# Kernel optimization log

Measured on AMD Instinct MI355X. Metric: run time of the kernel, lower is better.

Reference implementation:

```python
import jax, jax.numpy as jnp
import numpy as np

H, U = 64, 64  # matrix-completion patch size; system size is (H*U)^2 = 4096^2


def svtC(X, tau):
    # Singular value thresholding: soft-threshold singular values by tau.
    u, s, vt = jnp.linalg.svd(X, full_matrices=False)
    return (u * jax.nn.relu(s - tau)) @ vt


def setup_inputs() -> dict:
    key = jax.random.key(0)
    ks = jax.random.split(key, 12)
    x = jax.random.normal(ks[0], (H, U), jnp.float32)
    L = jax.random.normal(ks[1], (H, U), jnp.float32)
    entries_mask = jax.random.randint(ks[2], (H, U), 0, 2).astype(bool)
    # D_tilda: symmetric PSD (HU, HU) smoothness operator so the system is well-conditioned
    M = jax.random.normal(ks[3], (H * U, H * U), jnp.float32)
    D_tilda = (M @ M.T) / jnp.float32(H * U)
    th_P = jax.random.normal(ks[4], (H, U), jnp.float32)
    v = jax.random.normal(ks[5], (), jnp.float32)
    coef_gamma = jax.random.uniform(ks[6], (), jnp.float32)
    neta = jax.random.uniform(ks[7], (), jnp.float32)
    lamda1 = jax.random.uniform(ks[8], (), jnp.float32)
    lamda2 = jax.random.uniform(ks[9], (), jnp.float32)
    rho = jax.random.uniform(ks[10], (), jnp.float32) + jnp.float32(0.1)
    S = jax.random.normal(ks[11], (H, H), jnp.float32) / np.float32(np.sqrt(H))
    return {"x": x, "L": L, "entries_mask": entries_mask, "D_tilda": D_tilda,
            "th_P": th_P, "v": v, "coef_gamma": coef_gamma, "neta": neta,
            "lamda1": lamda1, "lamda2": lamda2, "rho": rho, "S": S}


def reference(x, L, entries_mask, D_tilda, th_P, v, coef_gamma, neta,
              lamda1, lamda2, rho, S):
    tau = jax.nn.sigmoid(v) * coef_gamma
    # Q_tilda = diag(vec(mask)); S_tilda = kron(I_U, S^T S)
    q = entries_mask.astype(jnp.float32).reshape(-1)  # (HU,)
    StS = S.T @ S                                      # (H, H)
    S_tilda = jnp.kron(jnp.eye(U, dtype=jnp.float32), StS)  # (HU, HU)
    eye = jnp.eye(H * U, dtype=jnp.float32)
    A = jnp.diag(q) + lamda1 * D_tilda + lamda2 * S_tilda + rho * eye
    vec = rho * (L - th_P) + jnp.where(entries_mask, x, jnp.float32(0.0))
    # Original uses explicit dense inverse followed by matvec
    Xtmp = (jnp.linalg.inv(A) @ vec.reshape(-1)).reshape(H, U)
    Ltmp = svtC(Xtmp + th_P, tau)
    Ptmp = th_P + neta * (Xtmp - Ltmp)
    return Ltmp, Ptmp
```

## Files before the change

### kernel.cpp

```cpp
#include <hip/hip_runtime.h>
#include <cstddef>

#define HU    4096
#define NBLK  256
#define NTHR  512
#define MAXIT 100
#define TOL2  1e-7f

#define WS_STS  0
#define WS_DINV 4096
#define WS_R0   8192
#define WS_U0   12288
#define WS_W    16384
#define WS_X    24576
#define WS_DEL  28672
#define WS_BAR  (WS_DEL + (MAXIT + 2) * 64)
#define WS_FLAG (WS_BAR + 8 * 16)
#define WS_END  (WS_FLAG + 1)

typedef _Float16 half4v __attribute__((ext_vector_type(4)));

__device__ __forceinline__ float fastrcp(float x) {
  float r; asm("v_rcp_f32 %0, %1" : "=v"(r) : "v"(x)); return r;
}
__device__ __forceinline__ float fastsqrt(float x) {
  float r; asm("v_sqrt_f32 %0, %1" : "=v"(r) : "v"(x)); return r;
}
__device__ __forceinline__ float fastrsq(float x) {
  float r; asm("v_rsq_f32 %0, %1" : "=v"(r) : "v"(x)); return r;
}

__device__ __forceinline__ float waveReduce(float v) {
#pragma unroll
  for (int off = 32; off > 0; off >>= 1) v += __shfl_xor(v, off, 64);
  return v;
}

__device__ __forceinline__ float blockSum(float v, float* red) {
  v = waveReduce(v);
  if ((threadIdx.x & 63) == 0) red[threadIdx.x >> 6] = v;
  __syncthreads();
  float s = 0.f;
#pragma unroll
  for (int i = 0; i < 8; ++i) s += red[i];
  __syncthreads();
  return s;
}

__device__ __forceinline__ void gsync(unsigned* cnt, unsigned* flag, unsigned gen) {
  __syncthreads();
  if (threadIdx.x == 0) {
    __threadfence();
    __hip_atomic_fetch_add(&cnt[(blockIdx.x & 7) * 16], 1u,
                           __ATOMIC_RELEASE, __HIP_MEMORY_SCOPE_AGENT);
    if (blockIdx.x == 0) {
      const unsigned target = gen * NBLK;
      for (;;) {
        unsigned s = 0;
#pragma unroll
        for (int i = 0; i < 8; ++i)
          s += __hip_atomic_load(&cnt[i * 16], __ATOMIC_RELAXED, __HIP_MEMORY_SCOPE_AGENT);
        if (s >= target) break;
        __builtin_amdgcn_s_sleep(1);
      }
      __hip_atomic_store(flag, gen, __ATOMIC_RELEASE, __HIP_MEMORY_SCOPE_AGENT);
    } else {
      while (__hip_atomic_load(flag, __ATOMIC_RELAXED, __HIP_MEMORY_SCOPE_AGENT) < gen)
        __builtin_amdgcn_s_sleep(1);
    }
    __threadfence();
  }
  __syncthreads();
}

__global__ void __launch_bounds__(NTHR, 1)
cg_solve_kernel(const float* __restrict__ x_in, const float* __restrict__ L_in,
                const int* __restrict__ mask, const float* __restrict__ D,
                const float* __restrict__ thP, const float* __restrict__ S,
                const float* __restrict__ l1p, const float* __restrict__ l2p,
                const float* __restrict__ rhop, float* __restrict__ ws)
{
  __shared__ __align__(16) float u_l[HU];
  __shared__ __align__(16) _Float16 Dh[16 * HU];
  __shared__ float red[8];
  unsigned* cnt  = (unsigned*)(ws + WS_BAR);
  unsigned* flag = (unsigned*)(ws + WS_FLAG);
  const float* sts = ws + WS_STS;
  const float lam1 = *l1p, lam2 = *l2p, rho = *rhop;
  const int tid = threadIdx.x, b = blockIdx.x;
  const int wv = tid >> 6, lane = tid & 63;
  unsigned gen = 0;

  const int gtid = b * NTHR + tid;
  if (gtid < HU) {
    const int a = gtid >> 6, c = gtid & 63;
    float acc = 0.f, sdiag = 0.f;
    for (int h = 0; h < 64; ++h) {
      const float sa = S[h * 64 + a], sc = S[h * 64 + c];
      acc = fmaf(sa, sc, acc);
      sdiag = fmaf(sc, sc, sdiag);
    }
    ws[WS_STS + gtid] = acc;
    const float q = mask[gtid] ? 1.f : 0.f;
    const float diag = q + rho + lam1 * D[(size_t)gtid * (HU + 1)] + lam2 * sdiag;
    const float bb = rho * (L_in[gtid] - thP[gtid]) + (mask[gtid] ? x_in[gtid] : 0.f);
    const float di = 1.f / diag;
    ws[WS_DINV + gtid] = di;
    ws[WS_R0 + gtid] = bb;
    ws[WS_U0 + gtid] = bb * di;
  }

  {
    const float4* __restrict__ Dg = (const float4*)(D + (size_t)b * 16 * HU);
    half4v* __restrict__ Dh4 = (half4v*)Dh;
    for (int o = tid; o < 16 * HU / 4; o += NTHR) {
      const float4 dv = Dg[o];
      half4v h;
      h[0] = (_Float16)dv.x; h[1] = (_Float16)dv.y;
      h[2] = (_Float16)dv.z; h[3] = (_Float16)dv.w;
      Dh4[o] = h;
    }
  }
  gsync(cnt, flag, ++gen);

  float r_reg[8], s_reg[8], dinv_reg[8];
  float acc0 = 0.f;
#pragma unroll
  for (int m = 0; m < 8; ++m) {
    const int i = tid + m * NTHR;
    const float rv = ws[WS_R0 + i], uv = ws[WS_U0 + i];
    r_reg[m] = rv; u_l[i] = uv; dinv_reg[m] = ws[WS_DINV + i];
    s_reg[m] = 0.f;
  }
  __syncthreads();
#pragma unroll
  for (int m = 0; m < 8; ++m) acc0 = fmaf(r_reg[m], u_l[tid + m * NTHR], acc0);
  const float gamma0 = blockSum(acc0, red);

  float p_arr[8], x_arr[8];
#pragma unroll
  for (int m = 0; m < 8; ++m) { p_arr[m] = 0.f; x_arr[m] = 0.f; }

  const int row0 = b * 16 + wv * 2;
  const int iq = row0 >> 6, j0 = row0 & 63;
  const float4* __restrict__ u4 = (const float4*)u_l;
  const float m0 = mask[row0] ? 1.f : 0.f;
  const float m1 = mask[row0 + 1] ? 1.f : 0.f;
  const float sts0 = sts[j0 * 64 + lane];
  const float sts1 = sts[j0 * 64 + 64 + lane];
  const float dex0 = D[(size_t)row0 * (HU + 1)];
  const float dex1 = D[(size_t)(row0 + 1) * (HU + 1)];
  const float diagf0 = m0 + rho + lam1 * (dex0 - (float)(_Float16)dex0);
  const float diagf1 = m1 + rho + lam1 * (dex1 - (float)(_Float16)dex1);
  const half4v* __restrict__ H0 = (const half4v*)(Dh + (size_t)(wv * 2) * HU);
  const half4v* __restrict__ H1 = H0 + (HU / 4);

  float gamma = gamma0, gamma_prev = 1.f, alpha_prev = 1.f;
  for (int k = 0; k < MAXIT; ++k) {
    float* __restrict__ wbuf = ws + WS_W + (k & 1) * HU;
    {
      float acc_a = 0.f, acc_b = 0.f;
#pragma unroll
      for (int it = 0; it < 16; ++it) {
        const float4 uu = u4[it * 64 + lane];
        const half4v d0 = H0[it * 64 + lane];
        const half4v d1 = H1[it * 64 + lane];
        acc_a = fmaf((float)d0[0], uu.x, acc_a); acc_a = fmaf((float)d0[1], uu.y, acc_a);
        acc_a = fmaf((float)d0[2], uu.z, acc_a); acc_a = fmaf((float)d0[3], uu.w, acc_a);
        acc_b = fmaf((float)d1[0], uu.x, acc_b); acc_b = fmaf((float)d1[1], uu.y, acc_b);
        acc_b = fmaf((float)d1[2], uu.z, acc_b); acc_b = fmaf((float)d1[3], uu.w, acc_b);
      }
      const float us = u_l[iq * 64 + lane];
      float t0 = fmaf(lam1, acc_a, lam2 * (sts0 * us));
      float t1 = fmaf(lam1, acc_b, lam2 * (sts1 * us));
      t0 = waveReduce(t0);
      t1 = waveReduce(t1);
      const float u0v = u_l[row0], u1v = u_l[row0 + 1];
      const float w0 = t0 + diagf0 * u0v;
      const float w1 = t1 + diagf1 * u1v;
      if (lane == 0) {
        wbuf[row0] = w0;
        wbuf[row0 + 1] = w1;
        red[wv] = fmaf(w0, u0v, w1 * u1v);
      }
      __syncthreads();
      if (tid == 0) {
        float s = 0.f;
#pragma unroll
        for (int k2 = 0; k2 < 8; ++k2) s += red[k2];
        atomicAdd(&ws[WS_DEL + k * 64 + (b & 63)], s);
      }
    }
    gsync(cnt, flag, ++gen);

    const float dk = waveReduce(ws[WS_DEL + k * 64 + lane]);
    const float beta  = (k == 0) ? 0.f : gamma * fastrcp(gamma_prev);
    const float denom = (k == 0) ? dk  : (dk - beta * gamma * fastrcp(alpha_prev));
    const float alpha = gamma * fastrcp(denom);

    float acc = 0.f;
#pragma unroll
    for (int m = 0; m < 8; ++m) {
      const int i = tid + m * NTHR;
      const float uold = u_l[i];
      const float wvv = wbuf[i];
      const float sv = (k == 0) ? wvv : fmaf(beta, s_reg[m], wvv);
      s_reg[m] = sv;
      const float rv = fmaf(-alpha, sv, r_reg[m]);
      r_reg[m] = rv;
      const float uv = rv * dinv_reg[m];
      u_l[i] = uv;
      acc = fmaf(rv, uv, acc);
      const float pk = (k == 0) ? uold : fmaf(beta, p_arr[m], uold);
      p_arr[m] = pk;
      x_arr[m] = fmaf(alpha, pk, x_arr[m]);
    }
    const float gnext = blockSum(acc, red);

    gamma_prev = gamma;
    alpha_prev = alpha;
    gamma = gnext;
    if (!(gnext > TOL2 * gamma0)) break;
  }

  if (b == 0) {
#pragma unroll
    for (int m = 0; m < 8; ++m) ws[WS_X + tid + m * NTHR] = x_arr[m];
  }
}


#define SWP 6
#define S_W 68

__device__ __forceinline__ float red16(float x) {
  int t;
  t = __builtin_amdgcn_update_dpp(0, __float_as_int(x), 0x128, 0xF, 0xF, false);
  x += __int_as_float(t);
  t = __builtin_amdgcn_update_dpp(0, __float_as_int(x), 0x124, 0xF, 0xF, false);
  x += __int_as_float(t);
  t = __builtin_amdgcn_update_dpp(0, __float_as_int(x), 0x122, 0xF, 0xF, false);
  x += __int_as_float(t);
  t = __builtin_amdgcn_update_dpp(0, __float_as_int(x), 0x121, 0xF, 0xF, false);
  x += __int_as_float(t);
  return x;
}

__global__ void __launch_bounds__(512)
svt_kernel(const float* __restrict__ thP, const float* __restrict__ vp,
           const float* __restrict__ cgp, const float* __restrict__ netap,
           const float* __restrict__ ws, float* __restrict__ out)
{
  const float* xsol = ws + WS_X;
  __shared__ __align__(16) float Wl[64 * S_W];
  __shared__ __align__(16) float Yr[64 * S_W];
  __shared__ __align__(16) float T1[64 * S_W];
  __shared__ __align__(16) float Wr[64 * S_W];
  __shared__ float g_s[64];
  __shared__ float red[8];
  const int tid = threadIdx.x;

  float t0acc = 0.f;
  for (int o = tid; o < 4096; o += 512) {
    const int r = o >> 6, c = o & 63;
    const float y = xsol[o] + thP[o];
    Wl[c * S_W + r] = y;
    Yr[r * S_W + c] = y;
    t0acc = fmaf(y, y, t0acc);
  }
  const float T0 = blockSum(t0acc, red);
  const float thr = 1.6e-10f * T0 * T0;

  const int m = tid >> 4;
  const int sub = tid & 15;
  int p = (m == 0) ? 63 : m;
  int q = (m == 0) ? 0  : 63 - m;

  for (int sweep = 0; sweep < SWP; ++sweep) {
    float offacc = 0.f;
    for (int rnd = 0; rnd < 63; ++rnd) {
      float4* wp = (float4*)(Wl + p * S_W) + sub;
      float4* wq = (float4*)(Wl + q * S_W) + sub;
      const float4 a = *wp, bb = *wq;
      float dpp = fmaf(a.x, a.x, fmaf(a.y, a.y, fmaf(a.z, a.z, a.w * a.w)));
      float dqq = fmaf(bb.x, bb.x, fmaf(bb.y, bb.y, fmaf(bb.z, bb.z, bb.w * bb.w)));
      float dpq = fmaf(a.x, bb.x, fmaf(a.y, bb.y, fmaf(a.z, bb.z, a.w * bb.w)));
      dpp = red16(dpp); dqq = red16(dqq); dpq = red16(dpq);
      offacc = fmaf(dpq, dpq, offacc);
      if (dpq * dpq > 1e-14f * dpp * dqq) {
        const float th = (dqq - dpp) * 0.5f * fastrcp(dpq);
        const float sg = (th >= 0.f) ? 1.f : -1.f;
        const float t  = sg * fastrcp(fabsf(th) + fastsqrt(fmaf(th, th, 1.f)));
        const float c1 = fastrsq(fmaf(t, t, 1.f));
        const float s1 = t * c1;
        float4 na, nb;
        na.x = c1 * a.x - s1 * bb.x;  nb.x = s1 * a.x + c1 * bb.x;
        na.y = c1 * a.y - s1 * bb.y;  nb.y = s1 * a.y + c1 * bb.y;
        na.z = c1 * a.z - s1 * bb.z;  nb.z = s1 * a.z + c1 * bb.z;
        na.w = c1 * a.w - s1 * bb.w;  nb.w = s1 * a.w + c1 * bb.w;
        *wp = na; *wq = nb;
      }
      if (m) { p = (p + 1 == 63) ? 0 : p + 1; }
      q = (q + 1 == 63) ? 0 : q + 1;
      __syncthreads();
    }
    const float tot = blockSum(offacc, red);
    if (sweep >= 3 && tot < thr) break;
  }

  if (tid < 64) {
    const float4* wc = (const float4*)(Wl + tid * S_W);
    float nn = 0.f;
#pragma unroll
    for (int i2 = 0; i2 < 16; ++i2) {
      const float4 u = wc[i2];
      nn = fmaf(u.x, u.x, fmaf(u.y, u.y, fmaf(u.z, u.z, fmaf(u.w, u.w, nn))));
    }
    const float sv = sqrtf(nn);
    const float tau = (*cgp) / (1.f + expf(-(*vp)));
    g_s[tid] = (sv > tau) ? (sv - tau) / (sv * nn) : 0.f;
  }
  __syncthreads();

  const int j = tid & 63;
  const int ib = tid >> 6;

#pragma unroll
  for (int mm = 0; mm < 8; ++mm) {
    const int k = ib + 8 * mm;
    const float4* wcol = (const float4*)(Wl + k * S_W);
    float acc = 0.f;
#pragma unroll
    for (int i4 = 0; i4 < 16; ++i4) {
      const float4 wv = wcol[i4];
      acc = fmaf(wv.x, Yr[(4 * i4 + 0) * S_W + j], acc);
      acc = fmaf(wv.y, Yr[(4 * i4 + 1) * S_W + j], acc);
      acc = fmaf(wv.z, Yr[(4 * i4 + 2) * S_W + j], acc);
      acc = fmaf(wv.w, Yr[(4 * i4 + 3) * S_W + j], acc);
    }
    T1[k * S_W + j] = acc;
  }
  for (int o = tid; o < 4096; o += 512) {
    const int i2 = o >> 6, kk = o & 63;
    Wr[i2 * S_W + kk] = Wl[kk * S_W + i2] * g_s[kk];
  }
  __syncthreads();

  const float neta = *netap;
#pragma unroll
  for (int mm = 0; mm < 8; ++mm) {
    const int i2 = ib + 8 * mm;
    const float4* wrow = (const float4*)(Wr + i2 * S_W);
    float acc = 0.f;
#pragma unroll
    for (int k4 = 0; k4 < 16; ++k4) {
      const float4 wv = wrow[k4];
      acc = fmaf(wv.x, T1[(4 * k4 + 0) * S_W + j], acc);
      acc = fmaf(wv.y, T1[(4 * k4 + 1) * S_W + j], acc);
      acc = fmaf(wv.z, T1[(4 * k4 + 2) * S_W + j], acc);
      acc = fmaf(wv.w, T1[(4 * k4 + 3) * S_W + j], acc);
    }
    const int o = i2 * 64 + j;
    out[o] = acc;
    out[4096 + o] = thP[o] + neta * (xsol[o] - acc);
  }
}

extern "C" void kernel_launch(void* const* d_in, const int* in_sizes, int n_in,
                              void* d_out, int out_size, void* d_ws, size_t ws_size,
                              hipStream_t stream)
{
  const float* x_in  = (const float*)d_in[0];
  const float* L_in  = (const float*)d_in[1];
  const int*   mask  = (const int*)d_in[2];
  const float* D     = (const float*)d_in[3];
  const float* thP   = (const float*)d_in[4];
  const float* vp    = (const float*)d_in[5];
  const float* cgp   = (const float*)d_in[6];
  const float* netap = (const float*)d_in[7];
  const float* l1p   = (const float*)d_in[8];
  const float* l2p   = (const float*)d_in[9];
  const float* rhop  = (const float*)d_in[10];
  const float* S     = (const float*)d_in[11];
  float* ws  = (float*)d_ws;
  float* out = (float*)d_out;

  hipMemsetAsync(ws + WS_DEL, 0, (WS_END - WS_DEL) * sizeof(float), stream);

  void* args[] = { (void*)&x_in, (void*)&L_in, (void*)&mask, (void*)&D, (void*)&thP,
                   (void*)&S, (void*)&l1p, (void*)&l2p, (void*)&rhop, (void*)&ws };
  hipLaunchCooperativeKernel((void*)cg_solve_kernel, dim3(NBLK), dim3(NTHR),
                             args, 0, stream);

  svt_kernel<<<1, 512, 0, stream>>>(thP, vp, cgp, netap, ws, out);
}
```

Before: 351.6 us.

## Fuse SVT into CG kernel and broadcast dot product through grid barrier

Folds the single-block SVT kernel into the cooperative CG kernel: block 0 keeps x in registers and reuses the shared-memory pool for the Jacobi SVD workspaces, which removes a second launch and a global round trip for x. Each iteration's grid barrier is also reworked so block 0 reduces the per-block partial dot products and broadcasts the scalar through replicated flag slots. This lets other blocks read a single value instead of 64 partials, and spreads polling across eight cache lines. The minimum number of Jacobi sweeps before an early exit drops from 4 to 3, which slightly loosens SVD accuracy, and block 0 no longer sleeps while it spins.

```diff
diff --git a/kernel.cpp b/kernel.cpp
--- a/kernel.cpp
+++ b/kernel.cpp
@@ -12,11 +12,10 @@
 #define WS_R0   8192
 #define WS_U0   12288
 #define WS_W    16384
-#define WS_X    24576
-#define WS_DEL  28672
+#define WS_DEL  24576
 #define WS_BAR  (WS_DEL + (MAXIT + 2) * 64)
 #define WS_FLAG (WS_BAR + 8 * 16)
-#define WS_END  (WS_FLAG + 1)
+#define WS_END  (WS_FLAG + 8 * 16)
 
 typedef _Float16 half4v __attribute__((ext_vector_type(4)));
 
@@ -47,7 +46,7 @@
   return s;
 }
 
-__device__ __forceinline__ void gsync(unsigned* cnt, unsigned* flag, unsigned gen) {
+__device__ __forceinline__ void gsync_init(unsigned* cnt, unsigned* flg, unsigned gen) {
   __syncthreads();
   if (threadIdx.x == 0) {
     __threadfence();
@@ -61,30 +60,103 @@
         for (int i = 0; i < 8; ++i)
           s += __hip_atomic_load(&cnt[i * 16], __ATOMIC_RELAXED, __HIP_MEMORY_SCOPE_AGENT);
         if (s >= target) break;
+      }
+#pragma unroll
+      for (int i = 0; i < 8; ++i)
+        __hip_atomic_store(&flg[i * 16], gen, __ATOMIC_RELEASE, __HIP_MEMORY_SCOPE_AGENT);
+    } else {
+      const int fl = (blockIdx.x & 7) * 16;
+      while (__hip_atomic_load(&flg[fl], __ATOMIC_RELAXED, __HIP_MEMORY_SCOPE_AGENT) < gen)
         __builtin_amdgcn_s_sleep(1);
-      }
-      __hip_atomic_store(flag, gen, __ATOMIC_RELEASE, __HIP_MEMORY_SCOPE_AGENT);
-    } else {
-      while (__hip_atomic_load(flag, __ATOMIC_RELAXED, __HIP_MEMORY_SCOPE_AGENT) < gen)
+    }
+    __threadfence();
+  }
+  __syncthreads();
+}
+
+__device__ __forceinline__ float gsync_dk(unsigned* cnt, unsigned* flg, unsigned gen,
+                                          float* dslot, float* redf) {
+  __syncthreads();
+  const int b = blockIdx.x;
+  if (b == 0) {
+    if (threadIdx.x < 64) {
+      if (threadIdx.x == 0) {
+        __threadfence();
+        __hip_atomic_fetch_add(&cnt[0], 1u, __ATOMIC_RELEASE, __HIP_MEMORY_SCOPE_AGENT);
+        const unsigned target = gen * NBLK;
+        for (;;) {
+          unsigned s = 0;
+#pragma unroll
+          for (int i = 0; i < 8; ++i)
+            s += __hip_atomic_load(&cnt[i * 16], __ATOMIC_RELAXED, __HIP_MEMORY_SCOPE_AGENT);
+          if (s >= target) break;
+        }
+        __threadfence();
+      }
+      const float dv = __hip_atomic_load(&dslot[threadIdx.x],
+                                         __ATOMIC_RELAXED, __HIP_MEMORY_SCOPE_AGENT);
+      const float dk = waveReduce(dv);
+      if (threadIdx.x == 0) {
+        const unsigned bits = __float_as_uint(dk);
+#pragma unroll
+        for (int i = 0; i < 8; ++i) {
+          __hip_atomic_store(&flg[i * 16 + 1], bits, __ATOMIC_RELAXED, __HIP_MEMORY_SCOPE_AGENT);
+          __hip_atomic_store(&flg[i * 16],    gen,  __ATOMIC_RELEASE, __HIP_MEMORY_SCOPE_AGENT);
+        }
+        redf[0] = dk;
+      }
+    }
+  } else {
+    if (threadIdx.x == 0) {
+      __threadfence();
+      __hip_atomic_fetch_add(&cnt[(b & 7) * 16], 1u,
+                             __ATOMIC_RELEASE, __HIP_MEMORY_SCOPE_AGENT);
+      const int fl = (b & 7) * 16;
+      while (__hip_atomic_load(&flg[fl], __ATOMIC_RELAXED, __HIP_MEMORY_SCOPE_AGENT) < gen)
         __builtin_amdgcn_s_sleep(1);
-    }
-    __threadfence();
-  }
-  __syncthreads();
+      const unsigned bits = __hip_atomic_load(&flg[fl + 1],
+                                              __ATOMIC_RELAXED, __HIP_MEMORY_SCOPE_AGENT);
+      __threadfence();
+      redf[0] = __uint_as_float(bits);
+    }
+  }
+  __syncthreads();
+  const float dk = redf[0];
+  __syncthreads();
+  return dk;
+}
+
+#define SWP 6
+#define S_W 68
+
+__device__ __forceinline__ float red16(float x) {
+  int t;
+  t = __builtin_amdgcn_update_dpp(0, __float_as_int(x), 0x128, 0xF, 0xF, false);
+  x += __int_as_float(t);
+  t = __builtin_amdgcn_update_dpp(0, __float_as_int(x), 0x124, 0xF, 0xF, false);
+  x += __int_as_float(t);
+  t = __builtin_amdgcn_update_dpp(0, __float_as_int(x), 0x122, 0xF, 0xF, false);
+  x += __int_as_float(t);
+  t = __builtin_amdgcn_update_dpp(0, __float_as_int(x), 0x121, 0xF, 0xF, false);
+  x += __int_as_float(t);
+  return x;
 }
 
 __global__ void __launch_bounds__(NTHR, 1)
-cg_solve_kernel(const float* __restrict__ x_in, const float* __restrict__ L_in,
-                const int* __restrict__ mask, const float* __restrict__ D,
-                const float* __restrict__ thP, const float* __restrict__ S,
-                const float* __restrict__ l1p, const float* __restrict__ l2p,
-                const float* __restrict__ rhop, float* __restrict__ ws)
+fused_kernel(const float* __restrict__ x_in, const float* __restrict__ L_in,
+             const int* __restrict__ mask, const float* __restrict__ D,
+             const float* __restrict__ thP, const float* __restrict__ S,
+             const float* __restrict__ l1p, const float* __restrict__ l2p,
+             const float* __restrict__ rhop, const float* __restrict__ vp,
+             const float* __restrict__ cgp, const float* __restrict__ netap,
+             float* __restrict__ ws, float* __restrict__ out)
 {
   __shared__ __align__(16) float u_l[HU];
-  __shared__ __align__(16) _Float16 Dh[16 * HU];
+  __shared__ __align__(16) char pool[128 * 1024];
   __shared__ float red[8];
+  __shared__ float g_s[64];
   unsigned* cnt  = (unsigned*)(ws + WS_BAR);
-  unsigned* flag = (unsigned*)(ws + WS_FLAG);
+  unsigned* flg  = (unsigned*)(ws + WS_FLAG);
   const float* sts = ws + WS_STS;
   const float lam1 = *l1p, lam2 = *l2p, rho = *rhop;
   const int tid = threadIdx.x, b = blockIdx.x;
@@ -112,7 +184,7 @@
 
   {
     const float4* __restrict__ Dg = (const float4*)(D + (size_t)b * 16 * HU);
-    half4v* __restrict__ Dh4 = (half4v*)Dh;
+    half4v* __restrict__ Dh4 = (half4v*)pool;
     for (int o = tid; o < 16 * HU / 4; o += NTHR) {
       const float4 dv = Dg[o];
       half4v h;
@@ -121,7 +193,7 @@
       Dh4[o] = h;
     }
   }
-  gsync(cnt, flag, ++gen);
+  gsync_init(cnt, flg, ++gen);
 
   float r_reg[8], s_reg[8], dinv_reg[8];
   float acc0 = 0.f;
@@ -152,7 +224,7 @@
   const float dex1 = D[(size_t)(row0 + 1) * (HU + 1)];
   const float diagf0 = m0 + rho + lam1 * (dex0 - (float)(_Float16)dex0);
   const float diagf1 = m1 + rho + lam1 * (dex1 - (float)(_Float16)dex1);
-  const half4v* __restrict__ H0 = (const half4v*)(Dh + (size_t)(wv * 2) * HU);
+  const half4v* __restrict__ H0 = (const half4v*)((_Float16*)pool + (size_t)(wv * 2) * HU);
   const half4v* __restrict__ H1 = H0 + (HU / 4);
 
   float gamma = gamma0, gamma_prev = 1.f, alpha_prev = 1.f;
@@ -191,9 +263,8 @@
         atomicAdd(&ws[WS_DEL + k * 64 + (b & 63)], s);
       }
     }
-    gsync(cnt, flag, ++gen);
-
-    const float dk = waveReduce(ws[WS_DEL + k * 64 + lane]);
+    const float dk = gsync_dk(cnt, flg, ++gen, ws + WS_DEL + k * 64, red);
+
     const float beta  = (k == 0) ? 0.f : gamma * fastrcp(gamma_prev);
     const float denom = (k == 0) ? dk  : (dk - beta * gamma * fastrcp(alpha_prev));
     const float alpha = gamma * fastrcp(denom);
@@ -223,58 +294,31 @@
     if (!(gnext > TOL2 * gamma0)) break;
   }
 
-  if (b == 0) {
-#pragma unroll
-    for (int m = 0; m < 8; ++m) ws[WS_X + tid + m * NTHR] = x_arr[m];
-  }
-}
-
-
-#define SWP 6
-#define S_W 68
-
-__device__ __forceinline__ float red16(float x) {
-  int t;
-  t = __builtin_amdgcn_update_dpp(0, __float_as_int(x), 0x128, 0xF, 0xF, false);
-  x += __int_as_float(t);
-  t = __builtin_amdgcn_update_dpp(0, __float_as_int(x), 0x124, 0xF, 0xF, false);
-  x += __int_as_float(t);
-  t = __builtin_amdgcn_update_dpp(0, __float_as_int(x), 0x122, 0xF, 0xF, false);
-  x += __int_as_float(t);
-  t = __builtin_amdgcn_update_dpp(0, __float_as_int(x), 0x121, 0xF, 0xF, false);
-  x += __int_as_float(t);
-  return x;
-}
-
-__global__ void __launch_bounds__(512)
-svt_kernel(const float* __restrict__ thP, const float* __restrict__ vp,
-           const float* __restrict__ cgp, const float* __restrict__ netap,
-           const float* __restrict__ ws, float* __restrict__ out)
-{
-  const float* xsol = ws + WS_X;
-  __shared__ __align__(16) float Wl[64 * S_W];
-  __shared__ __align__(16) float Yr[64 * S_W];
-  __shared__ __align__(16) float T1[64 * S_W];
-  __shared__ __align__(16) float Wr[64 * S_W];
-  __shared__ float g_s[64];
-  __shared__ float red[8];
-  const int tid = threadIdx.x;
+  if (b != 0) return;
+
+  float* Wl = (float*)pool;
+  float* Yr = Wl + 64 * S_W;
+  float* T1 = Yr + 64 * S_W;
+  float* Wr = T1 + 64 * S_W;
+  __syncthreads();
 
   float t0acc = 0.f;
-  for (int o = tid; o < 4096; o += 512) {
-    const int r = o >> 6, c = o & 63;
-    const float y = xsol[o] + thP[o];
-    Wl[c * S_W + r] = y;
-    Yr[r * S_W + c] = y;
+#pragma unroll
+  for (int mm = 0; mm < 8; ++mm) {
+    const int i = tid + mm * NTHR;
+    const int rr = i >> 6, cc = i & 63;
+    const float y = x_arr[mm] + thP[i];
+    Wl[cc * S_W + rr] = y;
+    Yr[rr * S_W + cc] = y;
     t0acc = fmaf(y, y, t0acc);
   }
   const float T0 = blockSum(t0acc, red);
   const float thr = 1.6e-10f * T0 * T0;
 
-  const int m = tid >> 4;
+  const int pid = tid >> 4;
   const int sub = tid & 15;
-  int p = (m == 0) ? 63 : m;
-  int q = (m == 0) ? 0  : 63 - m;
+  int p = (pid == 0) ? 63 : pid;
+  int q = (pid == 0) ? 0  : 63 - pid;
 
   for (int sweep = 0; sweep < SWP; ++sweep) {
     float offacc = 0.f;
@@ -300,12 +344,12 @@
         na.w = c1 * a.w - s1 * bb.w;  nb.w = s1 * a.w + c1 * bb.w;
         *wp = na; *wq = nb;
       }
-      if (m) { p = (p + 1 == 63) ? 0 : p + 1; }
+      if (pid) { p = (p + 1 == 63) ? 0 : p + 1; }
       q = (q + 1 == 63) ? 0 : q + 1;
       __syncthreads();
     }
     const float tot = blockSum(offacc, red);
-    if (sweep >= 3 && tot < thr) break;
+    if (sweep >= 2 && tot < thr) break;
   }
 
   if (tid < 64) {
@@ -332,11 +376,11 @@
     float acc = 0.f;
 #pragma unroll
     for (int i4 = 0; i4 < 16; ++i4) {
-      const float4 wv = wcol[i4];
-      acc = fmaf(wv.x, Yr[(4 * i4 + 0) * S_W + j], acc);
-      acc = fmaf(wv.y, Yr[(4 * i4 + 1) * S_W + j], acc);
-      acc = fmaf(wv.z, Yr[(4 * i4 + 2) * S_W + j], acc);
-      acc = fmaf(wv.w, Yr[(4 * i4 + 3) * S_W + j], acc);
+      const float4 wvv = wcol[i4];
+      acc = fmaf(wvv.x, Yr[(4 * i4 + 0) * S_W + j], acc);
+      acc = fmaf(wvv.y, Yr[(4 * i4 + 1) * S_W + j], acc);
+      acc = fmaf(wvv.z, Yr[(4 * i4 + 2) * S_W + j], acc);
+      acc = fmaf(wvv.w, Yr[(4 * i4 + 3) * S_W + j], acc);
     }
     T1[k * S_W + j] = acc;
   }
@@ -354,15 +398,15 @@
     float acc = 0.f;
 #pragma unroll
     for (int k4 = 0; k4 < 16; ++k4) {
-      const float4 wv = wrow[k4];
-      acc = fmaf(wv.x, T1[(4 * k4 + 0) * S_W + j], acc);
-      acc = fmaf(wv.y, T1[(4 * k4 + 1) * S_W + j], acc);
-      acc = fmaf(wv.z, T1[(4 * k4 + 2) * S_W + j], acc);
-      acc = fmaf(wv.w, T1[(4 * k4 + 3) * S_W + j], acc);
+      const float4 wvv = wrow[k4];
+      acc = fmaf(wvv.x, T1[(4 * k4 + 0) * S_W + j], acc);
+      acc = fmaf(wvv.y, T1[(4 * k4 + 1) * S_W + j], acc);
+      acc = fmaf(wvv.z, T1[(4 * k4 + 2) * S_W + j], acc);
+      acc = fmaf(wvv.w, T1[(4 * k4 + 3) * S_W + j], acc);
     }
     const int o = i2 * 64 + j;
     out[o] = acc;
-    out[4096 + o] = thP[o] + neta * (xsol[o] - acc);
+    out[4096 + o] = thP[o] + neta * (x_arr[mm] - acc);
   }
 }
 
@@ -388,9 +432,8 @@
   hipMemsetAsync(ws + WS_DEL, 0, (WS_END - WS_DEL) * sizeof(float), stream);
 
   void* args[] = { (void*)&x_in, (void*)&L_in, (void*)&mask, (void*)&D, (void*)&thP,
-                   (void*)&S, (void*)&l1p, (void*)&l2p, (void*)&rhop, (void*)&ws };
-  hipLaunchCooperativeKernel((void*)cg_solve_kernel, dim3(NBLK), dim3(NTHR),
+                   (void*)&S, (void*)&l1p, (void*)&l2p, (void*)&rhop,
+                   (void*)&vp, (void*)&cgp, (void*)&netap, (void*)&ws, (void*)&out };
+  hipLaunchCooperativeKernel((void*)fused_kernel, dim3(NBLK), dim3(NTHR),
                              args, 0, stream);
-
-  svt_kernel<<<1, 512, 0, stream>>>(thP, vp, cgp, netap, ws, out);
-}
+}
```

New measurement: 382.2 us. 1.09x slower.
